# Optimization experiments

Hardware: AMD Instinct MI355X
Metric: run time of the kernel (lower is better)

Reference implementation:

```python
import jax, jax.numpy as jnp
import numpy as np

HEADS = 16
D_MODEL = 2048
HEAD_DIM = D_MODEL // HEADS


def setup_inputs() -> dict:
    key = jax.random.key(0)
    ks = jax.random.split(key, 8)
    s = 1.0 / np.sqrt(D_MODEL)
    return {
        "hidden_states": jax.random.normal(ks[0], (2, 2048, D_MODEL), jnp.float32),
        "Wq": jax.random.normal(ks[1], (D_MODEL, D_MODEL), jnp.float32) * s,
        "bq": jax.random.normal(ks[2], (D_MODEL,), jnp.float32) * s,
        "Wk": jax.random.normal(ks[3], (D_MODEL, D_MODEL), jnp.float32) * s,
        "Wv": jax.random.normal(ks[4], (D_MODEL, D_MODEL), jnp.float32) * s,
        "bv": jax.random.normal(ks[5], (D_MODEL,), jnp.float32) * s,
        "Wo": jax.random.normal(ks[6], (D_MODEL, D_MODEL), jnp.float32) * s,
        "bo": jax.random.normal(ks[7], (D_MODEL,), jnp.float32) * s,
    }


def reference(hidden_states, Wq, bq, Wk, Wv, bv, Wo, bo):
    bsz, q_len, _ = hidden_states.shape
    # torch Linear: y = x @ W^T + b; k_W has no bias
    q = hidden_states @ Wq.T + bq
    k = hidden_states @ Wk.T
    v = hidden_states @ Wv.T + bv
    # [b, h, s, d]
    def split_heads(t):
        return t.reshape(bsz, q_len, HEADS, HEAD_DIM).transpose(0, 2, 1, 3)
    q, k, v = split_heads(q), split_heads(k), split_heads(v)
    scale = 1.0 / np.sqrt(HEAD_DIM).astype(np.float32)
    attn_weights = jnp.einsum("bhqd,bhkd->bhqk", q, k) * scale
    attn_weights = jax.nn.softmax(attn_weights, axis=-1)
    attn_output = jnp.einsum("bhqk,bhkd->bhqd", attn_weights, v)
    attn_output = attn_output.transpose(0, 2, 1, 3).reshape(bsz, q_len, D_MODEL)
    attn_output = attn_output @ Wo.T + bo
    return attn_output, attn_weights
```

## Files before the change

kernel.cpp:

```cpp
#include <hip/hip_runtime.h>

typedef _Float16 f16;
typedef _Float16 f16x4 __attribute__((ext_vector_type(4)));
typedef _Float16 f16x8 __attribute__((ext_vector_type(8)));
typedef float f32x4 __attribute__((ext_vector_type(4)));

#define DM 2048
#define NT 4096
#define SEQ 2048
#define HD 128
#define NBH 32
#define QSCALE (0.08838834764831845f * 1.4426950408889634f)

__device__ __forceinline__ void gload16(const f16* g, f16* l) {
  __builtin_amdgcn_global_load_lds(
      (const __attribute__((address_space(1))) void*)g,
      (__attribute__((address_space(3))) void*)l, 16, 0, 0);
}

#define LGKM0                                         \
  asm volatile("s_waitcnt lgkmcnt(0)" ::: "memory"); \
  __builtin_amdgcn_sched_barrier(0)
#define VMC6                                         \
  asm volatile("s_waitcnt vmcnt(6)" ::: "memory");   \
  __builtin_amdgcn_sched_barrier(0)
#define VMC0                                         \
  asm volatile("s_waitcnt vmcnt(0)" ::: "memory");   \
  __builtin_amdgcn_sched_barrier(0)

__global__ __launch_bounds__(256) void cvt_f32_f16(const float* __restrict__ src,
                                                   f16* __restrict__ dst, int n4) {
  int i = blockIdx.x * 256 + threadIdx.x;
  int st = gridDim.x * 256;
  for (; i < n4; i += st) {
    float4 v = ((const float4*)src)[i];
    f16x4 h = {(f16)v.x, (f16)v.y, (f16)v.z, (f16)v.w};
    ((f16x4*)dst)[i] = h;
  }
}

__global__ __launch_bounds__(256) void cvt3_f32_f16(const float* __restrict__ s0,
                                                    const float* __restrict__ s1,
                                                    const float* __restrict__ s2,
                                                    f16* __restrict__ dst) {
  int i = blockIdx.x * 256 + threadIdx.x;
  int st = gridDim.x * 256;
  for (; i < 3 * 1048576; i += st) {
    const int r = i >> 20, j = i & 1048575;
    const float* s = (r == 0) ? s0 : ((r == 1) ? s1 : s2);
    float4 v = ((const float4*)s)[j];
    f16x4 h = {(f16)v.x, (f16)v.y, (f16)v.z, (f16)v.w};
    ((f16x4*)dst)[i] = h;
  }
}

template <int MODE>
__global__ __launch_bounds__(512, 2) void gemm8(const f16* __restrict__ A,
                                                const f16* __restrict__ Bm,
                                                const float* __restrict__ bias1,
                                                const float* __restrict__ bias2,
                                                float* __restrict__ outF,
                                                f16* __restrict__ outQ,
                                                f16* __restrict__ outK,
                                                f16* __restrict__ outV) {
  __shared__ __align__(16) f16 smem[73728];
  const int tid = threadIdx.x;
  const int w = tid >> 6, l = tid & 63;
  const int wr = w >> 2, wc = w & 3;
  const int sl = l & 15, t4 = l >> 4;

  const int nbx = gridDim.x;
  const int flat = blockIdx.y * nbx + blockIdx.x;
  const int chunk = (nbx * gridDim.y) >> 3;
  const int swz = (flat & 7) * chunk + (flat >> 3);
  const int row0 = (swz / nbx) * 128, col0 = (swz % nbx) * 256;

  f32x4 acc[4][4] = {};

  const int sr8 = l >> 3;
  const int sch = (l & 7) ^ (sr8 & 7);
  const f16* gA0 = A + (size_t)(row0 + w * 8 + sr8) * DM + sch * 8;
  const f16* gB0 = Bm + (size_t)(col0 + w * 8 + sr8) * DM + sch * 8;

#define SA(tb, kt, r) \
  gload16(gA0 + (size_t)(r) * 64 * DM + (kt) * 64, smem + (tb) * 8192 + (r) * 4096 + w * 512)
#define SB(tb, kt, r)                                  \
  gload16(gB0 + (size_t)(r) * 64 * DM + (kt) * 64,    \
          smem + 24576 + (tb) * 16384 + (r) * 4096 + w * 512)
#define MF(mi, ni, av, bv) \
  acc[mi][ni] = __builtin_amdgcn_mfma_f32_16x16x32_f16(av, bv, acc[mi][ni], 0, 0, 0)

  const int sx = sl & 7;
  const int sk0 = (t4 ^ sx) * 8;
  const int sk1 = ((4 + t4) ^ sx) * 8;
  const int arow = (wr * 64 + sl) * 64;
  const int brow = (wc * 64 + sl) * 64;

  SA(0, 0, 0); SA(0, 0, 1);
  SB(0, 0, 0); SB(0, 0, 1); SB(0, 0, 2); SB(0, 0, 3);
  SA(1, 1, 0); SA(1, 1, 1);
  SB(1, 1, 0); SB(1, 1, 1); SB(1, 1, 2); SB(1, 1, 3);
  VMC6;
  __builtin_amdgcn_s_barrier();

  int cur = 0;
#pragma unroll 1
  for (int t = 0; t < 32; ++t) {
    const int nb = (cur == 0) ? 2 : cur - 1;
    const bool pf = (t + 2 < 32);
    const int ab = cur * 8192;
    const int bb = 24576 + cur * 16384;
    f16x8 b0, b1, b2, b3, a0, a1;

    b0 = *(const f16x8*)&smem[bb + brow + sk0];
    b1 = *(const f16x8*)&smem[bb + brow + 1024 + sk0];
    b2 = *(const f16x8*)&smem[bb + brow + 2048 + sk0];
    b3 = *(const f16x8*)&smem[bb + brow + 3072 + sk0];
    a0 = *(const f16x8*)&smem[ab + arow + sk0];
    a1 = *(const f16x8*)&smem[ab + arow + 1024 + sk0];
    if (pf) { SA(nb, t + 2, 0); SA(nb, t + 2, 1); }
    __builtin_amdgcn_s_barrier();
    LGKM0;
    __builtin_amdgcn_s_setprio(1);
    MF(0, 0, a0, b0); MF(0, 1, a0, b1); MF(0, 2, a0, b2); MF(0, 3, a0, b3);
    MF(1, 0, a1, b0); MF(1, 1, a1, b1); MF(1, 2, a1, b2); MF(1, 3, a1, b3);
    __builtin_amdgcn_s_setprio(0);
    __builtin_amdgcn_s_barrier();

    a0 = *(const f16x8*)&smem[ab + arow + 2048 + sk0];
    a1 = *(const f16x8*)&smem[ab + arow + 3072 + sk0];
    if (pf) { SB(nb, t + 2, 0); SB(nb, t + 2, 1); }
    __builtin_amdgcn_s_barrier();
    LGKM0;
    __builtin_amdgcn_s_setprio(1);
    MF(2, 0, a0, b0); MF(2, 1, a0, b1); MF(2, 2, a0, b2); MF(2, 3, a0, b3);
    MF(3, 0, a1, b0); MF(3, 1, a1, b1); MF(3, 2, a1, b2); MF(3, 3, a1, b3);
    __builtin_amdgcn_s_setprio(0);
    __builtin_amdgcn_s_barrier();

    b0 = *(const f16x8*)&smem[bb + brow + sk1];
    b1 = *(const f16x8*)&smem[bb + brow + 1024 + sk1];
    b2 = *(const f16x8*)&smem[bb + brow + 2048 + sk1];
    b3 = *(const f16x8*)&smem[bb + brow + 3072 + sk1];
    a0 = *(const f16x8*)&smem[ab + arow + sk1];
    a1 = *(const f16x8*)&smem[ab + arow + 1024 + sk1];
    if (pf) { SB(nb, t + 2, 2); SB(nb, t + 2, 3); }
    __builtin_amdgcn_s_barrier();
    LGKM0;
    __builtin_amdgcn_s_setprio(1);
    MF(0, 0, a0, b0); MF(0, 1, a0, b1); MF(0, 2, a0, b2); MF(0, 3, a0, b3);
    MF(1, 0, a1, b0); MF(1, 1, a1, b1); MF(1, 2, a1, b2); MF(1, 3, a1, b3);
    __builtin_amdgcn_s_setprio(0);
    __builtin_amdgcn_s_barrier();

    a0 = *(const f16x8*)&smem[ab + arow + 2048 + sk1];
    a1 = *(const f16x8*)&smem[ab + arow + 3072 + sk1];
    __builtin_amdgcn_s_barrier();
    LGKM0;
    __builtin_amdgcn_s_setprio(1);
    MF(2, 0, a0, b0); MF(2, 1, a0, b1); MF(2, 2, a0, b2); MF(2, 3, a0, b3);
    MF(3, 0, a1, b0); MF(3, 1, a1, b1); MF(3, 2, a1, b2); MF(3, 3, a1, b3);
    __builtin_amdgcn_s_setprio(0);
    if (t < 30) { VMC6; } else { VMC0; }
    __builtin_amdgcn_s_barrier();
    cur = (cur == 2) ? 0 : cur + 1;
  }
#undef SA
#undef SB
#undef MF

  const int rl0 = wr * 64 + t4 * 4;
  const int cl0 = wc * 64 + sl;
  if constexpr (MODE == 0) {
#pragma unroll
    for (int mi = 0; mi < 4; mi++) {
#pragma unroll
      for (int ni = 0; ni < 4; ni++) {
        const int col = col0 + cl0 + ni * 16;
        const float bi = bias1[col];
#pragma unroll
        for (int j = 0; j < 4; j++) {
          const int row = row0 + rl0 + mi * 16 + j;
          outF[(size_t)row * DM + col] = acc[mi][ni][j] + bi;
        }
      }
    }
  } else {
    const int region = col0 >> 11;
    const int c2 = col0 & 2047;
    __syncthreads();
    if (region == 2) {
#pragma unroll
      for (int mi = 0; mi < 4; mi++)
#pragma unroll
        for (int ni = 0; ni < 4; ni++) {
          const int cl = cl0 + ni * 16;
          const float bb2 = bias2[c2 + cl];
#pragma unroll
          for (int j = 0; j < 4; j++)
            smem[cl * 136 + rl0 + mi * 16 + j] = (f16)(acc[mi][ni][j] + bb2);
        }
      __syncthreads();
      const int b = row0 >> 11, s0 = row0 & 2047;
#pragma unroll
      for (int it = 0; it < 8; ++it) {
        const int ck = it * 512 + tid;
        const int ci = ck >> 4, cc = (ck & 15) * 8;
        const int dg = c2 + ci;
        *(f16x8*)&outV[((size_t)(b * 16 + (dg >> 7)) * HD + (dg & 127)) * SEQ + s0 + cc] =
            *(const f16x8*)&smem[ci * 136 + cc];
      }
    } else {
#pragma unroll
      for (int mi = 0; mi < 4; mi++)
#pragma unroll
        for (int ni = 0; ni < 4; ni++) {
          const int cl = cl0 + ni * 16;
          const int cg = c2 + cl;
          const float badd = (region == 0) ? bias1[cg] : 0.0f;
#pragma unroll
          for (int j = 0; j < 4; j++) {
            float v = acc[mi][ni][j] + badd;
            if (region == 0) v *= QSCALE;
            smem[(rl0 + mi * 16 + j) * 264 + cl] = (f16)v;
          }
        }
      __syncthreads();
      f16* const dst = (region == 0 ? outQ : outK) + (size_t)row0 * DM + c2;
#pragma unroll
      for (int it = 0; it < 8; ++it) {
        const int ck = it * 512 + tid;
        const int rr = ck >> 5, cc = (ck & 31) * 8;
        *(f16x8*)&dst[(size_t)rr * DM + cc] = *(const f16x8*)&smem[rr * 264 + cc];
      }
    }
  }
}

__global__ __launch_bounds__(256, 2) void attn(const f16* __restrict__ Q,
                                               const f16* __restrict__ Kt,
                                               const f16* __restrict__ Vt,
                                               float* __restrict__ Pout,
                                               f16* __restrict__ Oout) {
  __shared__ __align__(16) f16 smem[36864];
  f16* const lP = smem + 32768;

  const int tid = threadIdx.x, w = tid >> 6, l = tid & 63;
  const int t = l >> 4, sl = l & 15, t8 = l >> 3, sl8 = l & 7;

  const int flat = blockIdx.y * gridDim.x + blockIdx.x;
  const int swz = (flat & 7) * 128 + (flat >> 3);
  const int bh = swz >> 5, q0 = (swz & 31) * 64;

  const int b = bh >> 4, h = bh & 15;
  const f16* Qg = Q + (size_t)(b * SEQ) * DM + h * HD;
  const f16* Kg = Kt + (size_t)(b * SEQ) * DM + h * HD;
  const f16* Vg = Vt + (size_t)bh * HD * SEQ;

#pragma unroll
  for (int c = 0; c < 4; c++) {
    const int row = w * 16 + c * 4 + t;
    const int ch = sl ^ (row & 7);
    gload16(Qg + (size_t)(q0 + row) * DM + ch * 8, smem + 16384 + w * 2048 + c * 512);
    gload16(Kg + (size_t)row * DM + ch * 8, smem + w * 2048 + c * 512);
  }
  __syncthreads();

  f16x8 qf[4];
  {
    const int row = w * 16 + sl;
#pragma unroll
    for (int g = 0; g < 4; g++) {
      const int ch = (g * 4 + t) ^ (row & 7);
      qf[g] = *(const f16x8*)&smem[16384 + row * 128 + ch * 8];
    }
  }

  float lsum = 0.0f;

  for (int kb = 0; kb < 32; ++kb) {
    f16* const kc = smem + (kb & 1) * 8192;
    if (kb < 31) {
      f16* const kn = smem + ((kb + 1) & 1) * 8192;
#pragma unroll
      for (int c = 0; c < 4; c++) {
        const int row = w * 16 + c * 4 + t;
        const int ch = sl ^ (row & 7);
        gload16(Kg + (size_t)((kb + 1) * 64 + row) * DM + ch * 8, kn + w * 2048 + c * 512);
      }
    }
#pragma unroll
    for (int cb = 0; cb < 4; ++cb) {
      f32x4 s = {0.f, 0.f, 0.f, 0.f};
      const int key = cb * 16 + sl;
#pragma unroll
      for (int g = 0; g < 4; ++g) {
        const int ch = (g * 4 + t) ^ (key & 7);
        f16x8 kf = *(const f16x8*)&kc[key * 128 + ch * 8];
        s = __builtin_amdgcn_mfma_f32_16x16x32_f16(kf, qf[g], s, 0, 0, 0);
      }
#pragma unroll
      for (int j = 0; j < 4; j++) lsum += __builtin_amdgcn_exp2f(s[j]);
    }
    __syncthreads();
  }
  lsum += __shfl_xor(lsum, 16);
  lsum += __shfl_xor(lsum, 32);
  const float inv = 1.0f / lsum;

  {
#pragma unroll
    for (int c = 0; c < 4; c++) {
      const int row = w * 16 + c * 4 + t;
      const int ch = sl ^ (row & 7);
      gload16(Kg + (size_t)row * DM + ch * 8, smem + w * 2048 + c * 512);
    }
#pragma unroll
    for (int c = 0; c < 4; c++) {
      const int row = w * 32 + c * 8 + t8;
      const int ch = sl8 ^ (row & 7);
      gload16(Vg + (size_t)row * SEQ + ch * 8, smem + 16384 + w * 2048 + c * 512);
    }
  }
  __syncthreads();

  f32x4 oacc[8] = {};
  const int qrow = w * 16 + sl;
  float* const Prow = Pout + ((size_t)bh * SEQ + q0 + qrow) * SEQ;

  for (int kb = 0; kb < 32; ++kb) {
    f16* const kc = smem + (kb & 1) * 8192;
    f16* const vc = smem + 16384 + (kb & 1) * 8192;
    if (kb < 31) {
      f16* const kn = smem + ((kb + 1) & 1) * 8192;
      f16* const vn = smem + 16384 + ((kb + 1) & 1) * 8192;
#pragma unroll
      for (int c = 0; c < 4; c++) {
        const int row = w * 16 + c * 4 + t;
        const int ch = sl ^ (row & 7);
        gload16(Kg + (size_t)((kb + 1) * 64 + row) * DM + ch * 8, kn + w * 2048 + c * 512);
      }
#pragma unroll
      for (int c = 0; c < 4; c++) {
        const int row = w * 32 + c * 8 + t8;
        const int ch = sl8 ^ (row & 7);
        gload16(Vg + (size_t)row * SEQ + (kb + 1) * 64 + ch * 8, vn + w * 2048 + c * 512);
      }
    }
#pragma unroll
    for (int cb = 0; cb < 4; ++cb) {
      f32x4 s = {0.f, 0.f, 0.f, 0.f};
      const int key = cb * 16 + sl;
#pragma unroll
      for (int g = 0; g < 4; ++g) {
        const int ch = (g * 4 + t) ^ (key & 7);
        f16x8 kf = *(const f16x8*)&kc[key * 128 + ch * 8];
        s = __builtin_amdgcn_mfma_f32_16x16x32_f16(kf, qf[g], s, 0, 0, 0);
      }
      f32x4 p4;
      f16x4 ph;
#pragma unroll
      for (int j = 0; j < 4; j++) {
        const float p = __builtin_amdgcn_exp2f(s[j]) * inv;
        p4[j] = p;
        ph[j] = (f16)p;
      }
      __builtin_nontemporal_store(p4, (f32x4*)(Prow + kb * 64 + cb * 16 + t * 4));
      const int chs = (cb * 2 + (t >> 1)) ^ (qrow & 7);
      *(f16x4*)&lP[qrow * 64 + chs * 8 + (t & 1) * 4] = ph;
    }
    f16x8 pf[2];
#pragma unroll
    for (int ks = 0; ks < 2; ++ks) {
      const int ch = (ks * 4 + t) ^ (qrow & 7);
      pf[ks] = *(const f16x8*)&lP[qrow * 64 + ch * 8];
    }
    __builtin_amdgcn_s_setprio(1);
#pragma unroll
    for (int cb = 0; cb < 8; ++cb) {
      const int d = cb * 16 + sl;
#pragma unroll
      for (int ks = 0; ks < 2; ++ks) {
        const int ch = (ks * 4 + t) ^ (d & 7);
        f16x8 vf = *(const f16x8*)&vc[d * 64 + ch * 8];
        oacc[cb] = __builtin_amdgcn_mfma_f32_16x16x32_f16(pf[ks], vf, oacc[cb], 0, 0, 0);
      }
    }
    __builtin_amdgcn_s_setprio(0);
    __syncthreads();
  }

#pragma unroll
  for (int cb = 0; cb < 8; ++cb) {
    const int d = cb * 16 + sl;
#pragma unroll
    for (int j = 0; j < 4; j++) {
      const int lrow = w * 16 + t * 4 + j;
      Oout[((size_t)(b * SEQ + q0 + lrow)) * DM + h * HD + d] = (f16)oacc[cb][j];
    }
  }
}

extern "C" void kernel_launch(void* const* d_in, const int* in_sizes, int n_in,
                              void* d_out, int out_size, void* d_ws, size_t ws_size,
                              hipStream_t stream) {
  const float* hs = (const float*)d_in[0];
  const float* Wq = (const float*)d_in[1];
  const float* bq = (const float*)d_in[2];
  const float* Wk = (const float*)d_in[3];
  const float* Wv = (const float*)d_in[4];
  const float* bv = (const float*)d_in[5];
  const float* Wo = (const float*)d_in[6];
  const float* bo = (const float*)d_in[7];
  float* out = (float*)d_out;
  float* Pout = out + (size_t)NT * DM;

  f16* q16 = (f16*)d_ws;
  f16* k16 = q16 + (size_t)NT * DM;
  f16* vt16 = k16 + (size_t)NT * DM;
  f16* ao16 = vt16 + (size_t)NT * DM;
  f16* hs16 = (f16*)Pout;
  f16* wqkv16 = hs16 + (size_t)NT * DM;
  f16* wo16 = q16;

  cvt_f32_f16<<<2048, 256, 0, stream>>>(hs, hs16, NT * DM / 4);
  cvt3_f32_f16<<<2048, 256, 0, stream>>>(Wq, Wk, Wv, wqkv16);

  gemm8<3><<<dim3(6144 / 256, NT / 128), 512, 0, stream>>>(
      hs16, wqkv16, bq, bv, nullptr, q16, k16, vt16);

  attn<<<dim3(SEQ / 64, NBH), 256, 0, stream>>>(q16, k16, vt16, Pout, ao16);

  cvt_f32_f16<<<1024, 256, 0, stream>>>(Wo, wo16, DM * DM / 4);
  gemm8<0><<<dim3(DM / 256, NT / 128), 512, 0, stream>>>(
      ao16, wo16, bo, nullptr, out, nullptr, nullptr, nullptr);
}
```

Measured before the change: 388.4 us.

## Deepen attention K prefetch to two stages and fuse input conversion kernels

The attention row-sum pass now keeps K tiles in four LDS buffers and prefetches two blocks ahead. The full __syncthreads at the end of each iteration becomes a partial vmcnt wait plus a barrier, so global loads can overlap compute for longer. The second pass also switches to a vmcnt(4) wait plus barrier. The hidden-state and QKV weight conversions are merged into one launch to save a kernel launch. The partial vmcnt waits depend on exact outstanding-load counts, so any miscount could cause races.

Result: faster. 379.9 us (-2.2%).

```diff
diff --git a/kernel.cpp b/kernel.cpp
--- a/kernel.cpp
+++ b/kernel.cpp
@@ -18,14 +18,17 @@
       (__attribute__((address_space(3))) void*)l, 16, 0, 0);
 }
 
-#define LGKM0                                         \
+#define LGKM0                                        \
   asm volatile("s_waitcnt lgkmcnt(0)" ::: "memory"); \
   __builtin_amdgcn_sched_barrier(0)
-#define VMC6                                         \
-  asm volatile("s_waitcnt vmcnt(6)" ::: "memory");   \
+#define VMC6                                       \
+  asm volatile("s_waitcnt vmcnt(6)" ::: "memory"); \
   __builtin_amdgcn_sched_barrier(0)
-#define VMC0                                         \
-  asm volatile("s_waitcnt vmcnt(0)" ::: "memory");   \
+#define VMC4                                       \
+  asm volatile("s_waitcnt vmcnt(4)" ::: "memory"); \
+  __builtin_amdgcn_sched_barrier(0)
+#define VMC0                                       \
+  asm volatile("s_waitcnt vmcnt(0)" ::: "memory"); \
   __builtin_amdgcn_sched_barrier(0)
 
 __global__ __launch_bounds__(256) void cvt_f32_f16(const float* __restrict__ src,
@@ -39,18 +42,29 @@
   }
 }
 
-__global__ __launch_bounds__(256) void cvt3_f32_f16(const float* __restrict__ s0,
+__global__ __launch_bounds__(256) void cvt4_f32_f16(const float* __restrict__ hs,
+                                                    const float* __restrict__ s0,
                                                     const float* __restrict__ s1,
                                                     const float* __restrict__ s2,
-                                                    f16* __restrict__ dst) {
+                                                    f16* __restrict__ hsd,
+                                                    f16* __restrict__ wd) {
   int i = blockIdx.x * 256 + threadIdx.x;
   int st = gridDim.x * 256;
-  for (; i < 3 * 1048576; i += st) {
-    const int r = i >> 20, j = i & 1048575;
-    const float* s = (r == 0) ? s0 : ((r == 1) ? s1 : s2);
-    float4 v = ((const float4*)s)[j];
-    f16x4 h = {(f16)v.x, (f16)v.y, (f16)v.z, (f16)v.w};
-    ((f16x4*)dst)[i] = h;
+  for (; i < 5 * 1048576; i += st) {
+    float4 v;
+    f16x4 h;
+    if (i < 2 * 1048576) {
+      v = ((const float4*)hs)[i];
+      h[0] = (f16)v.x; h[1] = (f16)v.y; h[2] = (f16)v.z; h[3] = (f16)v.w;
+      ((f16x4*)hsd)[i] = h;
+    } else {
+      const int j = i - 2 * 1048576;
+      const int r = j >> 20, jj = j & 1048575;
+      const float* s = (r == 0) ? s0 : ((r == 1) ? s1 : s2);
+      v = ((const float4*)s)[jj];
+      h[0] = (f16)v.x; h[1] = (f16)v.y; h[2] = (f16)v.z; h[3] = (f16)v.w;
+      ((f16x4*)wd)[j] = h;
+    }
   }
 }
 
@@ -84,8 +98,8 @@
 
 #define SA(tb, kt, r) \
   gload16(gA0 + (size_t)(r) * 64 * DM + (kt) * 64, smem + (tb) * 8192 + (r) * 4096 + w * 512)
-#define SB(tb, kt, r)                                  \
-  gload16(gB0 + (size_t)(r) * 64 * DM + (kt) * 64,    \
+#define SB(tb, kt, r)                               \
+  gload16(gB0 + (size_t)(r) * 64 * DM + (kt) * 64, \
           smem + 24576 + (tb) * 16384 + (r) * 4096 + w * 512)
 #define MF(mi, ni, av, bv) \
   acc[mi][ni] = __builtin_amdgcn_mfma_f32_16x16x32_f16(av, bv, acc[mi][ni], 0, 0, 0)
@@ -263,6 +277,7 @@
     const int ch = sl ^ (row & 7);
     gload16(Qg + (size_t)(q0 + row) * DM + ch * 8, smem + 16384 + w * 2048 + c * 512);
     gload16(Kg + (size_t)row * DM + ch * 8, smem + w * 2048 + c * 512);
+    gload16(Kg + (size_t)(64 + row) * DM + ch * 8, smem + 8192 + w * 2048 + c * 512);
   }
   __syncthreads();
 
@@ -275,18 +290,20 @@
       qf[g] = *(const f16x8*)&smem[16384 + row * 128 + ch * 8];
     }
   }
+  LGKM0;
+  __builtin_amdgcn_s_barrier();
 
   float lsum = 0.0f;
 
   for (int kb = 0; kb < 32; ++kb) {
-    f16* const kc = smem + (kb & 1) * 8192;
-    if (kb < 31) {
-      f16* const kn = smem + ((kb + 1) & 1) * 8192;
+    f16* const kc = smem + (kb & 3) * 8192;
+    if (kb + 2 < 32) {
+      f16* const kn = smem + ((kb + 2) & 3) * 8192;
 #pragma unroll
       for (int c = 0; c < 4; c++) {
         const int row = w * 16 + c * 4 + t;
         const int ch = sl ^ (row & 7);
-        gload16(Kg + (size_t)((kb + 1) * 64 + row) * DM + ch * 8, kn + w * 2048 + c * 512);
+        gload16(Kg + (size_t)((kb + 2) * 64 + row) * DM + ch * 8, kn + w * 2048 + c * 512);
       }
     }
 #pragma unroll
@@ -302,7 +319,10 @@
 #pragma unroll
       for (int j = 0; j < 4; j++) lsum += __builtin_amdgcn_exp2f(s[j]);
     }
-    __syncthreads();
+    if (kb < 31) {
+      if (kb + 2 < 32) { VMC4; } else { VMC0; }
+      __builtin_amdgcn_s_barrier();
+    }
   }
   lsum += __shfl_xor(lsum, 16);
   lsum += __shfl_xor(lsum, 32);
@@ -387,7 +407,10 @@
       }
     }
     __builtin_amdgcn_s_setprio(0);
-    __syncthreads();
+    if (kb < 31) {
+      VMC4;
+      __builtin_amdgcn_s_barrier();
+    }
   }
 
 #pragma unroll
@@ -423,8 +446,7 @@
   f16* wqkv16 = hs16 + (size_t)NT * DM;
   f16* wo16 = q16;
 
-  cvt_f32_f16<<<2048, 256, 0, stream>>>(hs, hs16, NT * DM / 4);
-  cvt3_f32_f16<<<2048, 256, 0, stream>>>(Wq, Wk, Wv, wqkv16);
+  cvt4_f32_f16<<<2048, 256, 0, stream>>>(hs, Wq, Wk, Wv, hs16, wqkv16);
 
   gemm8<3><<<dim3(6144 / 256, NT / 128), 512, 0, stream>>>(
       hs16, wqkv16, bq, bv, nullptr, q16, k16, vt16);
```
